# Kernel optimization log

Hardware: AMD Instinct MI355X
Metric: run time of the kernel (lower is better)

## Reference

```python
import jax, jax.numpy as jnp
import numpy as np

# SC encoding (reconstructed from the module's scaling identity):
#   x (float) is normalized by leftShift so that ax * 2**ls is in [2**(dW-1), 2**dW)
#   the bitstream encodes q = floor(ax * 2**ls * L / 2**dW) ones: bit[t] = (rngSeq[t] < q)
#   so x ~= popcount(bits) * 2**(dW - ls - log2 L)   (matches test_1 in the source)
# BitstreamMUL: product = popcount(b1 & b2) * 2**(2*dW - ls1 - ls2 - log2 L)
# (tensor_2 uses the ascending sequence => thermometer code, so AND-popcount is a dot product)


def _gen_bitstreams(x, seq, dataWidth, L):
    ax = jnp.abs(x)
    sign = jnp.where(x > 0, 1.0, -1.0)            # source: sign = 1 if >0 else -1
    nz = (ax > 0).astype(x.dtype)                 # Zero flag (inverted)
    safe = jnp.where(ax > 0, ax, 1.0)
    ls = dataWidth - 1.0 - jnp.floor(jnp.log2(safe))   # normalize to [2**(dW-1), 2**dW)
    scaled = ax * jnp.exp2(ls)
    q = jnp.floor(scaled * (L / (2.0 ** dataWidth)))   # number of ones in bitstream
    bits = (seq[None, None, :].astype(x.dtype) < q[..., None]).astype(x.dtype)
    bits = bits * nz[..., None]
    return bits, ls, sign, nz


def setup_inputs() -> dict:
    key = jax.random.key(0)
    k1, k2 = jax.random.split(key)
    M, K, N, L = 512, 512, 512, 256
    tensor_1 = jax.random.normal(k1, (M, K), dtype=jnp.float32)
    tensor_2 = jax.random.normal(k2, (K, N), dtype=jnp.float32)
    rngSeq = jnp.arange(L, dtype=jnp.int32)  # LFSR permutation of 0..L-1; arange per spec
    return {"tensor_1": tensor_1, "tensor_2": tensor_2, "rngSeq": rngSeq, "dataWidth": 8}


def reference(tensor_1, tensor_2, rngSeq, dataWidth):
    L = rngSeq.shape[0]
    logL = float(np.log2(L))
    dW = float(dataWidth)

    b1, ls1, s1, nz1 = _gen_bitstreams(tensor_1, rngSeq, dW, L)          # [M,K,L]
    asc = jnp.arange(L, dtype=jnp.int32)                                  # ascendingSeq
    b2, ls2, s2, nz2 = _gen_bitstreams(tensor_2, asc, dW, L)             # [K,N,L]

    # fold per-element SC scale 2**(2dW - ls1 - ls2 - logL), sign, and Zero mask
    A = b1 * (s1 * nz1 * jnp.exp2(dW - ls1 - logL))[..., None]           # [M,K,L]
    B = b2 * (s2 * nz2 * jnp.exp2(dW - ls2))[..., None]                  # [K,N,L]

    M, K, _ = A.shape
    N = B.shape[1]
    # AND-popcount accumulate over (k, t) == single big GEMM over K*L
    approximateResult = A.reshape(M, K * L) @ B.transpose(0, 2, 1).reshape(K * L, N)
    exactResult = tensor_1 @ tensor_2
    return approximateResult, exactResult
```

## Files before the change

kernel.cpp:

```cpp
#include <hip/hip_runtime.h>
#include <math.h>

#define MDIM 512
#define NDIM 512
#define KDIM 512
#define MN (MDIM * NDIM)

#define BM 64
#define BN 64
#define BK 32
#define LSTR 68

__device__ __forceinline__ void sc_encode(float x, int shAdj, float Lf,
                                          float& v, float& q) {
    float ax = fabsf(x);
    v = 0.0f; q = 0.0f;
    if (ax > 0.0f) {
        int e;
        float m = frexpf(ax, &e);
        q = floorf(m * Lf);
        v = ldexpf((x > 0.0f) ? 1.0f : -1.0f, e + shAdj);
    }
}

template<int KS>
__global__ __launch_bounds__(256) void sc_gemm_k(
        const float* __restrict__ t1, const float* __restrict__ t2,
        float* __restrict__ dst, float Lf, int logL) {
    __shared__ __align__(16) float As_v[BK][LSTR];
    __shared__ __align__(16) float As_q[BK][LSTR];
    __shared__ __align__(16) float As_t[BK][LSTR];
    __shared__ __align__(16) float Bs_v[BK][LSTR];
    __shared__ __align__(16) float Bs_q[BK][LSTR];
    __shared__ __align__(16) float Bs_t[BK][LSTR];

    const int tid = threadIdx.x;
    const int tx = tid & 15;
    const int ty = tid >> 4;
    const int n0 = blockIdx.x * BN;
    const int m0 = blockIdx.y * BM;
    const int kbase = blockIdx.z * (KDIM / KS);

    float acc[4][4] = {};
    float acce[4][4] = {};

    for (int kt = 0; kt < (KDIM / KS) / BK; ++kt) {
        const int kk0 = kbase + kt * BK;
        if (kt) __syncthreads();

        #pragma unroll
        for (int ff = 0; ff < 2; ++ff) {
            int f = tid + ff * 256;
            int row = f >> 3;
            int c4  = (f & 7) << 2;
            float4 t = *(const float4*)(t1 + (m0 + row) * KDIM + kk0 + c4);
            const float* tp = &t.x;
            #pragma unroll
            for (int d = 0; d < 4; ++d) {
                float v, q;
                sc_encode(tp[d], -logL, Lf, v, q);
                As_v[c4 + d][row] = v;
                As_q[c4 + d][row] = q;
                As_t[c4 + d][row] = tp[d];
            }
        }
        #pragma unroll
        for (int ff = 0; ff < 2; ++ff) {
            int f = tid + ff * 256;
            int rowk = f >> 4;
            int c4   = (f & 15) << 2;
            float4 t = *(const float4*)(t2 + (kk0 + rowk) * NDIM + n0 + c4);
            float4 v4, q4;
            float* vp = &v4.x; float* qp = &q4.x; const float* tp = &t.x;
            #pragma unroll
            for (int d = 0; d < 4; ++d) sc_encode(tp[d], 0, Lf, vp[d], qp[d]);
            *(float4*)&Bs_v[rowk][c4] = v4;
            *(float4*)&Bs_q[rowk][c4] = q4;
            *(float4*)&Bs_t[rowk][c4] = t;
        }
        __syncthreads();

        #pragma unroll 8
        for (int kk = 0; kk < BK; ++kk) {
            float av[4], aq[4], at[4], bv[4], bq[4], bt[4];
            *(float4*)av = *(const float4*)&As_v[kk][ty << 2];
            *(float4*)aq = *(const float4*)&As_q[kk][ty << 2];
            *(float4*)at = *(const float4*)&As_t[kk][ty << 2];
            *(float4*)bv = *(const float4*)&Bs_v[kk][tx << 2];
            *(float4*)bq = *(const float4*)&Bs_q[kk][tx << 2];
            *(float4*)bt = *(const float4*)&Bs_t[kk][tx << 2];
            #pragma unroll
            for (int i = 0; i < 4; ++i) {
                #pragma unroll
                for (int j = 0; j < 4; ++j) {
                    acc[i][j]  = fmaf(av[i] * bv[j], fminf(aq[i], bq[j]), acc[i][j]);
                    acce[i][j] = fmaf(at[i], bt[j], acce[i][j]);
                }
            }
        }
    }

    float* o = dst + (size_t)blockIdx.z * (2 * MN);
    #pragma unroll
    for (int i = 0; i < 4; ++i) {
        int m = m0 + (ty << 2) + i;
        int nb = n0 + (tx << 2);
        float4 va = { acc[i][0],  acc[i][1],  acc[i][2],  acc[i][3] };
        float4 ve = { acce[i][0], acce[i][1], acce[i][2], acce[i][3] };
        *(float4*)&o[m * NDIM + nb]      = va;
        *(float4*)&o[MN + m * NDIM + nb] = ve;
    }
}

template<int KS>
__global__ __launch_bounds__(256) void reduce_k(const float4* __restrict__ ws,
                                                float4* __restrict__ out) {
    int i = blockIdx.x * blockDim.x + threadIdx.x;
    float4 s = ws[i];
    #pragma unroll
    for (int z = 1; z < KS; ++z) {
        float4 v = ws[(size_t)z * (2 * MN / 4) + i];
        s.x += v.x; s.y += v.y; s.z += v.z; s.w += v.w;
    }
    out[i] = s;
}

extern "C" void kernel_launch(void* const* d_in, const int* in_sizes, int n_in,
                              void* d_out, int out_size, void* d_ws, size_t ws_size,
                              hipStream_t stream) {
    const float* t1 = (const float*)d_in[0];
    const float* t2 = (const float*)d_in[1];
    int L = in_sizes[2];
    int logL = 31 - __builtin_clz((unsigned)L);
    float Lf = (float)L;

    float* out = (float*)d_out;
    float* ws  = (float*)d_ws;
    const size_t perSplit = (size_t)2 * MN * sizeof(float);
    const int nred = (2 * MN / 4) / 256;

    if (ws_size >= 8 * perSplit) {
        hipLaunchKernelGGL((sc_gemm_k<8>), dim3(NDIM / BN, MDIM / BM, 8), dim3(256),
                           0, stream, t1, t2, ws, Lf, logL);
        hipLaunchKernelGGL((reduce_k<8>), dim3(nred), dim3(256), 0, stream,
                           (const float4*)ws, (float4*)out);
    } else if (ws_size >= 4 * perSplit) {
        hipLaunchKernelGGL((sc_gemm_k<4>), dim3(NDIM / BN, MDIM / BM, 4), dim3(256),
                           0, stream, t1, t2, ws, Lf, logL);
        hipLaunchKernelGGL((reduce_k<4>), dim3(nred), dim3(256), 0, stream,
                           (const float4*)ws, (float4*)out);
    } else if (ws_size >= 2 * perSplit) {
        hipLaunchKernelGGL((sc_gemm_k<2>), dim3(NDIM / BN, MDIM / BM, 2), dim3(256),
                           0, stream, t1, t2, ws, Lf, logL);
        hipLaunchKernelGGL((reduce_k<2>), dim3(nred), dim3(256), 0, stream,
                           (const float4*)ws, (float4*)out);
    } else {
        hipLaunchKernelGGL((sc_gemm_k<1>), dim3(NDIM / BN, MDIM / BM, 1), dim3(256),
                           0, stream, t1, t2, out, Lf, logL);
    }
}
```

Before: 87.33 us.

## Use 8x8 register tiles with 64-thread blocks and 16-way split-K

```diff
diff --git a/kernel.cpp b/kernel.cpp
--- a/kernel.cpp
+++ b/kernel.cpp
@@ -8,7 +8,7 @@
 
 #define BM 64
 #define BN 64
-#define BK 32
+#define BK 16
 #define LSTR 68
 
 __device__ __forceinline__ void sc_encode(float x, int shAdj, float Lf,
@@ -24,7 +24,7 @@
 }
 
 template<int KS>
-__global__ __launch_bounds__(256) void sc_gemm_k(
+__global__ __launch_bounds__(64, 2) void sc_gemm_k(
         const float* __restrict__ t1, const float* __restrict__ t2,
         float* __restrict__ dst, float Lf, int logL) {
     __shared__ __align__(16) float As_v[BK][LSTR];
@@ -35,24 +35,24 @@
     __shared__ __align__(16) float Bs_t[BK][LSTR];
 
     const int tid = threadIdx.x;
-    const int tx = tid & 15;
-    const int ty = tid >> 4;
+    const int tx = tid & 7;
+    const int ty = tid >> 3;
     const int n0 = blockIdx.x * BN;
     const int m0 = blockIdx.y * BM;
     const int kbase = blockIdx.z * (KDIM / KS);
 
-    float acc[4][4] = {};
-    float acce[4][4] = {};
+    float acc[8][8] = {};
+    float acce[8][8] = {};
 
     for (int kt = 0; kt < (KDIM / KS) / BK; ++kt) {
         const int kk0 = kbase + kt * BK;
         if (kt) __syncthreads();
 
         #pragma unroll
-        for (int ff = 0; ff < 2; ++ff) {
-            int f = tid + ff * 256;
-            int row = f >> 3;
-            int c4  = (f & 7) << 2;
+        for (int ff = 0; ff < 4; ++ff) {
+            int f = tid + ff * 64;
+            int row = f >> 2;
+            int c4  = (f & 3) << 2;
             float4 t = *(const float4*)(t1 + (m0 + row) * KDIM + kk0 + c4);
             const float* tp = &t.x;
             #pragma unroll
@@ -65,8 +65,8 @@
             }
         }
         #pragma unroll
-        for (int ff = 0; ff < 2; ++ff) {
-            int f = tid + ff * 256;
+        for (int ff = 0; ff < 4; ++ff) {
+            int f = tid + ff * 64;
             int rowk = f >> 4;
             int c4   = (f & 15) << 2;
             float4 t = *(const float4*)(t2 + (kk0 + rowk) * NDIM + n0 + c4);
@@ -80,21 +80,28 @@
         }
         __syncthreads();
 
-        #pragma unroll 8
+        #pragma unroll 2
         for (int kk = 0; kk < BK; ++kk) {
-            float av[4], aq[4], at[4], bv[4], bq[4], bt[4];
-            *(float4*)av = *(const float4*)&As_v[kk][ty << 2];
-            *(float4*)aq = *(const float4*)&As_q[kk][ty << 2];
-            *(float4*)at = *(const float4*)&As_t[kk][ty << 2];
-            *(float4*)bv = *(const float4*)&Bs_v[kk][tx << 2];
-            *(float4*)bq = *(const float4*)&Bs_q[kk][tx << 2];
-            *(float4*)bt = *(const float4*)&Bs_t[kk][tx << 2];
+            float av[8], aq[8], at8[8], bv[8], bq[8], bt8[8];
+            const int a0 = ty << 3, b0 = tx << 3;
+            *(float4*)&av[0]  = *(const float4*)&As_v[kk][a0];
+            *(float4*)&av[4]  = *(const float4*)&As_v[kk][a0 + 4];
+            *(float4*)&aq[0]  = *(const float4*)&As_q[kk][a0];
+            *(float4*)&aq[4]  = *(const float4*)&As_q[kk][a0 + 4];
+            *(float4*)&at8[0] = *(const float4*)&As_t[kk][a0];
+            *(float4*)&at8[4] = *(const float4*)&As_t[kk][a0 + 4];
+            *(float4*)&bv[0]  = *(const float4*)&Bs_v[kk][b0];
+            *(float4*)&bv[4]  = *(const float4*)&Bs_v[kk][b0 + 4];
+            *(float4*)&bq[0]  = *(const float4*)&Bs_q[kk][b0];
+            *(float4*)&bq[4]  = *(const float4*)&Bs_q[kk][b0 + 4];
+            *(float4*)&bt8[0] = *(const float4*)&Bs_t[kk][b0];
+            *(float4*)&bt8[4] = *(const float4*)&Bs_t[kk][b0 + 4];
             #pragma unroll
-            for (int i = 0; i < 4; ++i) {
+            for (int i = 0; i < 8; ++i) {
                 #pragma unroll
-                for (int j = 0; j < 4; ++j) {
+                for (int j = 0; j < 8; ++j) {
                     acc[i][j]  = fmaf(av[i] * bv[j], fminf(aq[i], bq[j]), acc[i][j]);
-                    acce[i][j] = fmaf(at[i], bt[j], acce[i][j]);
+                    acce[i][j] = fmaf(at8[i], bt8[j], acce[i][j]);
                 }
             }
         }
@@ -102,13 +109,13 @@
 
     float* o = dst + (size_t)blockIdx.z * (2 * MN);
     #pragma unroll
-    for (int i = 0; i < 4; ++i) {
-        int m = m0 + (ty << 2) + i;
-        int nb = n0 + (tx << 2);
-        float4 va = { acc[i][0],  acc[i][1],  acc[i][2],  acc[i][3] };
-        float4 ve = { acce[i][0], acce[i][1], acce[i][2], acce[i][3] };
-        *(float4*)&o[m * NDIM + nb]      = va;
-        *(float4*)&o[MN + m * NDIM + nb] = ve;
+    for (int i = 0; i < 8; ++i) {
+        int m = m0 + (ty << 3) + i;
+        int nb = n0 + (tx << 3);
+        *(float4*)&o[m * NDIM + nb]          = *(float4*)&acc[i][0];
+        *(float4*)&o[m * NDIM + nb + 4]      = *(float4*)&acc[i][4];
+        *(float4*)&o[MN + m * NDIM + nb]     = *(float4*)&acce[i][0];
+        *(float4*)&o[MN + m * NDIM + nb + 4] = *(float4*)&acce[i][4];
     }
 }
 
@@ -139,23 +146,18 @@
     const size_t perSplit = (size_t)2 * MN * sizeof(float);
     const int nred = (2 * MN / 4) / 256;
 
-    if (ws_size >= 8 * perSplit) {
-        hipLaunchKernelGGL((sc_gemm_k<8>), dim3(NDIM / BN, MDIM / BM, 8), dim3(256),
+    if (ws_size >= 16 * perSplit) {
+        hipLaunchKernelGGL((sc_gemm_k<16>), dim3(NDIM / BN, MDIM / BM, 16), dim3(64),
+                           0, stream, t1, t2, ws, Lf, logL);
+        hipLaunchKernelGGL((reduce_k<16>), dim3(nred), dim3(256), 0, stream,
+                           (const float4*)ws, (float4*)out);
+    } else if (ws_size >= 8 * perSplit) {
+        hipLaunchKernelGGL((sc_gemm_k<8>), dim3(NDIM / BN, MDIM / BM, 8), dim3(64),
                            0, stream, t1, t2, ws, Lf, logL);
         hipLaunchKernelGGL((reduce_k<8>), dim3(nred), dim3(256), 0, stream,
                            (const float4*)ws, (float4*)out);
-    } else if (ws_size >= 4 * perSplit) {
-        hipLaunchKernelGGL((sc_gemm_k<4>), dim3(NDIM / BN, MDIM / BM, 4), dim3(256),
-                           0, stream, t1, t2, ws, Lf, logL);
-        hipLaunchKernelGGL((reduce_k<4>), dim3(nred), dim3(256), 0, stream,
-                           (const float4*)ws, (float4*)out);
-    } else if (ws_size >= 2 * perSplit) {
-        hipLaunchKernelGGL((sc_gemm_k<2>), dim3(NDIM / BN, MDIM / BM, 2), dim3(256),
-                           0, stream, t1, t2, ws, Lf, logL);
-        hipLaunchKernelGGL((reduce_k<2>), dim3(nred), dim3(256), 0, stream,
-                           (const float4*)ws, (float4*)out);
     } else {
-        hipLaunchKernelGGL((sc_gemm_k<1>), dim3(NDIM / BN, MDIM / BM, 1), dim3(256),
+        hipLaunchKernelGGL((sc_gemm_k<1>), dim3(NDIM / BN, MDIM / BM, 1), dim3(64),
                            0, stream, t1, t2, out, Lf, logL);
     }
 }
```

After: 93.73 us. 7.3% more time.

## Split exact GEMM into bf16 MFMA kernel and raise split-K for approximate GEMM

Applied to the files above, without the earlier changes.

```diff
diff --git a/kernel.cpp b/kernel.cpp
--- a/kernel.cpp
+++ b/kernel.cpp
@@ -1,4 +1,5 @@
 #include <hip/hip_runtime.h>
+#include <hip/hip_bf16.h>
 #include <math.h>
 
 #define MDIM 512
@@ -8,11 +9,14 @@
 
 #define BM 64
 #define BN 64
-#define BK 32
+#define BK 16
 #define LSTR 68
 
-__device__ __forceinline__ void sc_encode(float x, int shAdj, float Lf,
-                                          float& v, float& q) {
+typedef __attribute__((ext_vector_type(8))) short bf16x8;
+typedef __attribute__((ext_vector_type(4))) float f32x4;
+
+__device__ __forceinline__ void sc_encode_vq(float x, int shAdj, float Lf,
+                                             float& v, float& q) {
     float ax = fabsf(x);
     v = 0.0f; q = 0.0f;
     if (ax > 0.0f) {
@@ -24,15 +28,13 @@
 }
 
 template<int KS>
-__global__ __launch_bounds__(256) void sc_gemm_k(
+__global__ __launch_bounds__(256, 8) void approx_k(
         const float* __restrict__ t1, const float* __restrict__ t2,
         float* __restrict__ dst, float Lf, int logL) {
     __shared__ __align__(16) float As_v[BK][LSTR];
     __shared__ __align__(16) float As_q[BK][LSTR];
-    __shared__ __align__(16) float As_t[BK][LSTR];
     __shared__ __align__(16) float Bs_v[BK][LSTR];
     __shared__ __align__(16) float Bs_q[BK][LSTR];
-    __shared__ __align__(16) float Bs_t[BK][LSTR];
 
     const int tid = threadIdx.x;
     const int tx = tid & 15;
@@ -42,84 +44,129 @@
     const int kbase = blockIdx.z * (KDIM / KS);
 
     float acc[4][4] = {};
-    float acce[4][4] = {};
 
     for (int kt = 0; kt < (KDIM / KS) / BK; ++kt) {
         const int kk0 = kbase + kt * BK;
         if (kt) __syncthreads();
 
-        #pragma unroll
-        for (int ff = 0; ff < 2; ++ff) {
-            int f = tid + ff * 256;
-            int row = f >> 3;
-            int c4  = (f & 7) << 2;
+        {
+            int row = tid >> 2;
+            int c4  = (tid & 3) << 2;
             float4 t = *(const float4*)(t1 + (m0 + row) * KDIM + kk0 + c4);
             const float* tp = &t.x;
             #pragma unroll
             for (int d = 0; d < 4; ++d) {
                 float v, q;
-                sc_encode(tp[d], -logL, Lf, v, q);
+                sc_encode_vq(tp[d], -logL, Lf, v, q);
                 As_v[c4 + d][row] = v;
                 As_q[c4 + d][row] = q;
-                As_t[c4 + d][row] = tp[d];
             }
         }
-        #pragma unroll
-        for (int ff = 0; ff < 2; ++ff) {
-            int f = tid + ff * 256;
-            int rowk = f >> 4;
-            int c4   = (f & 15) << 2;
+        {
+            int rowk = tid >> 4;
+            int c4   = (tid & 15) << 2;
             float4 t = *(const float4*)(t2 + (kk0 + rowk) * NDIM + n0 + c4);
             float4 v4, q4;
             float* vp = &v4.x; float* qp = &q4.x; const float* tp = &t.x;
             #pragma unroll
-            for (int d = 0; d < 4; ++d) sc_encode(tp[d], 0, Lf, vp[d], qp[d]);
+            for (int d = 0; d < 4; ++d) sc_encode_vq(tp[d], 0, Lf, vp[d], qp[d]);
             *(float4*)&Bs_v[rowk][c4] = v4;
             *(float4*)&Bs_q[rowk][c4] = q4;
-            *(float4*)&Bs_t[rowk][c4] = t;
         }
         __syncthreads();
 
-        #pragma unroll 8
+        #pragma unroll 4
         for (int kk = 0; kk < BK; ++kk) {
-            float av[4], aq[4], at[4], bv[4], bq[4], bt[4];
+            float av[4], aq[4], bv[4], bq[4];
             *(float4*)av = *(const float4*)&As_v[kk][ty << 2];
             *(float4*)aq = *(const float4*)&As_q[kk][ty << 2];
-            *(float4*)at = *(const float4*)&As_t[kk][ty << 2];
             *(float4*)bv = *(const float4*)&Bs_v[kk][tx << 2];
             *(float4*)bq = *(const float4*)&Bs_q[kk][tx << 2];
-            *(float4*)bt = *(const float4*)&Bs_t[kk][tx << 2];
             #pragma unroll
             for (int i = 0; i < 4; ++i) {
                 #pragma unroll
                 for (int j = 0; j < 4; ++j) {
-                    acc[i][j]  = fmaf(av[i] * bv[j], fminf(aq[i], bq[j]), acc[i][j]);
-                    acce[i][j] = fmaf(at[i], bt[j], acce[i][j]);
+                    acc[i][j] = fmaf(av[i] * bv[j], fminf(aq[i], bq[j]), acc[i][j]);
                 }
             }
         }
     }
 
-    float* o = dst + (size_t)blockIdx.z * (2 * MN);
+    float* o = dst + (size_t)blockIdx.z * MN;
     #pragma unroll
     for (int i = 0; i < 4; ++i) {
         int m = m0 + (ty << 2) + i;
-        int nb = n0 + (tx << 2);
-        float4 va = { acc[i][0],  acc[i][1],  acc[i][2],  acc[i][3] };
-        float4 ve = { acce[i][0], acce[i][1], acce[i][2], acce[i][3] };
-        *(float4*)&o[m * NDIM + nb]      = va;
-        *(float4*)&o[MN + m * NDIM + nb] = ve;
+        float4 va = { acc[i][0], acc[i][1], acc[i][2], acc[i][3] };
+        *(float4*)&o[m * NDIM + n0 + (tx << 2)] = va;
+    }
+}
+
+__device__ __forceinline__ short bfbits(float x) {
+    union { __hip_bfloat16 h; short s; } u;
+    u.h = __float2bfloat16(x);
+    return u.s;
+}
+
+__device__ __forceinline__ bf16x8 cvt8_row(const float* p) {
+    float4 lo = *(const float4*)p;
+    float4 hi = *(const float4*)(p + 4);
+    bf16x8 r;
+    r[0] = bfbits(lo.x); r[1] = bfbits(lo.y); r[2] = bfbits(lo.z); r[3] = bfbits(lo.w);
+    r[4] = bfbits(hi.x); r[5] = bfbits(hi.y); r[6] = bfbits(hi.z); r[7] = bfbits(hi.w);
+    return r;
+}
+
+__device__ __forceinline__ bf16x8 cvt8_col(const float* p) {
+    bf16x8 r;
+    #pragma unroll
+    for (int j = 0; j < 8; ++j) r[j] = bfbits(p[j * NDIM]);
+    return r;
+}
+
+__global__ __launch_bounds__(256) void exact_mfma(
+        const float* __restrict__ t1, const float* __restrict__ t2,
+        float* __restrict__ out) {
+    const int w  = threadIdx.x >> 6;
+    const int l  = threadIdx.x & 63;
+    const int wr = w >> 1, wc = w & 1;
+    const int mb = blockIdx.y * 64 + wr * 32;
+    const int nb = blockIdx.x * 64 + wc * 32;
+    const int lr = l & 15;
+    const int kg = l >> 4;
+
+    f32x4 acc00 = {0,0,0,0}, acc01 = {0,0,0,0}, acc10 = {0,0,0,0}, acc11 = {0,0,0,0};
+
+    for (int k0 = 0; k0 < KDIM; k0 += 32) {
+        const int kb = k0 + kg * 8;
+        bf16x8 a0 = cvt8_row(t1 + (size_t)(mb + lr) * KDIM + kb);
+        bf16x8 a1 = cvt8_row(t1 + (size_t)(mb + 16 + lr) * KDIM + kb);
+        bf16x8 b0 = cvt8_col(t2 + (size_t)kb * NDIM + nb + lr);
+        bf16x8 b1 = cvt8_col(t2 + (size_t)kb * NDIM + nb + 16 + lr);
+        acc00 = __builtin_amdgcn_mfma_f32_16x16x32_bf16(a0, b0, acc00, 0, 0, 0);
+        acc01 = __builtin_amdgcn_mfma_f32_16x16x32_bf16(a0, b1, acc01, 0, 0, 0);
+        acc10 = __builtin_amdgcn_mfma_f32_16x16x32_bf16(a1, b0, acc10, 0, 0, 0);
+        acc11 = __builtin_amdgcn_mfma_f32_16x16x32_bf16(a1, b1, acc11, 0, 0, 0);
+    }
+
+    float* oe = out + MN;
+    #pragma unroll
+    for (int r = 0; r < 4; ++r) {
+        int r0 = mb + kg * 4 + r;
+        oe[(size_t)r0 * NDIM + nb + lr]             = acc00[r];
+        oe[(size_t)r0 * NDIM + nb + 16 + lr]        = acc01[r];
+        oe[(size_t)(r0 + 16) * NDIM + nb + lr]      = acc10[r];
+        oe[(size_t)(r0 + 16) * NDIM + nb + 16 + lr] = acc11[r];
     }
 }
 
 template<int KS>
-__global__ __launch_bounds__(256) void reduce_k(const float4* __restrict__ ws,
+__global__ __launch_bounds__(256) void reduce_a(const float4* __restrict__ ws,
                                                 float4* __restrict__ out) {
     int i = blockIdx.x * blockDim.x + threadIdx.x;
     float4 s = ws[i];
     #pragma unroll
     for (int z = 1; z < KS; ++z) {
-        float4 v = ws[(size_t)z * (2 * MN / 4) + i];
+        float4 v = ws[(size_t)z * (MN / 4) + i];
         s.x += v.x; s.y += v.y; s.z += v.z; s.w += v.w;
     }
     out[i] = s;
@@ -136,26 +183,29 @@
 
     float* out = (float*)d_out;
     float* ws  = (float*)d_ws;
-    const size_t perSplit = (size_t)2 * MN * sizeof(float);
-    const int nred = (2 * MN / 4) / 256;
-
-    if (ws_size >= 8 * perSplit) {
-        hipLaunchKernelGGL((sc_gemm_k<8>), dim3(NDIM / BN, MDIM / BM, 8), dim3(256),
+    const size_t slice = (size_t)MN * sizeof(float);
+    const int nred = (MN / 4) / 256;
+
+    hipLaunchKernelGGL(exact_mfma, dim3(NDIM / 64, MDIM / 64), dim3(256), 0,
+                       stream, t1, t2, out);
+
+    if (ws_size >= 32 * slice) {
+        hipLaunchKernelGGL((approx_k<32>), dim3(NDIM / BN, MDIM / BM, 32), dim3(256),
                            0, stream, t1, t2, ws, Lf, logL);
-        hipLaunchKernelGGL((reduce_k<8>), dim3(nred), dim3(256), 0, stream,
+        hipLaunchKernelGGL((reduce_a<32>), dim3(nred), dim3(256), 0, stream,
                            (const float4*)ws, (float4*)out);
-    } else if (ws_size >= 4 * perSplit) {
-        hipLaunchKernelGGL((sc_gemm_k<4>), dim3(NDIM / BN, MDIM / BM, 4), dim3(256),
+    } else if (ws_size >= 16 * slice) {
+        hipLaunchKernelGGL((approx_k<16>), dim3(NDIM / BN, MDIM / BM, 16), dim3(256),
                            0, stream, t1, t2, ws, Lf, logL);
-        hipLaunchKernelGGL((reduce_k<4>), dim3(nred), dim3(256), 0, stream,
+        hipLaunchKernelGGL((reduce_a<16>), dim3(nred), dim3(256), 0, stream,
                            (const float4*)ws, (float4*)out);
-    } else if (ws_size >= 2 * perSplit) {
-        hipLaunchKernelGGL((sc_gemm_k<2>), dim3(NDIM / BN, MDIM / BM, 2), dim3(256),
+    } else if (ws_size >= 8 * slice) {
+        hipLaunchKernelGGL((approx_k<8>), dim3(NDIM / BN, MDIM / BM, 8), dim3(256),
                            0, stream, t1, t2, ws, Lf, logL);
-        hipLaunchKernelGGL((reduce_k<2>), dim3(nred), dim3(256), 0, stream,
+        hipLaunchKernelGGL((reduce_a<8>), dim3(nred), dim3(256), 0, stream,
                            (const float4*)ws, (float4*)out);
     } else {
-        hipLaunchKernelGGL((sc_gemm_k<1>), dim3(NDIM / BN, MDIM / BM, 1), dim3(256),
+        hipLaunchKernelGGL((approx_k<1>), dim3(NDIM / BN, MDIM / BM, 1), dim3(256),
                            0, stream, t1, t2, out, Lf, logL);
     }
 }
```

Result: slower. 97.62 us (+11.8%).
